# Kernel tuning notes

Measured on AMD Instinct MI355X. Metric: run time of the kernel, lower is better.

The kernel has to match this reference:

```python
import jax, jax.numpy as jnp
import numpy as np

MAX_ITER = 10
F_TOL = 1e-8
FREE_NUM = 100  # free_idx[1] + 1
OUT_DIM = 512


def setup_inputs() -> dict:
    key = jax.random.key(0)
    ks = jax.random.split(key, 13)
    f32 = jnp.float32
    b = jax.random.normal(ks[0], (64, 448), f32)
    # MLP params (nn.Linear convention: W [out, in], bias [out])
    W1 = jax.random.normal(ks[1], (1024, 448), f32) * 0.05
    b1 = jax.random.normal(ks[2], (1024,), f32) * 0.01
    W2 = jax.random.normal(ks[3], (1024, 1024), f32) * 0.03
    b2 = jax.random.normal(ks[4], (1024,), f32) * 0.01
    W3 = jax.random.normal(ks[5], (1024, 1024), f32) * 0.03
    b3 = jax.random.normal(ks[6], (1024,), f32) * 0.01
    W4 = jax.random.normal(ks[7], (512, 1024), f32) * 0.03
    b4 = jax.random.normal(ks[8], (512,), f32) * 0.01
    A = jax.random.normal(ks[9], (448, 512), f32) * 0.05
    WzProj = jax.random.normal(ks[10], (512, 512), f32) * 0.01  # contractive
    WbProj = jax.random.normal(ks[11], (512, 448), f32) * 0.05
    return {"b": b, "W1": W1, "b1": b1, "W2": W2, "b2": b2, "W3": W3,
            "b3": b3, "W4": W4, "b4": b4, "A": A, "WzProj": WzProj,
            "WbProj": WbProj}


def _projection(out, b0, A, WzProj, WbProj):
    # Fixed-point projection with on-device convergence flag + Jacobian accum
    bsz = out.shape[0]
    Bias = b0 @ WbProj.T                     # [bsz, d]
    col = jnp.arange(OUT_DIM)
    J0 = jnp.broadcast_to(jnp.eye(OUT_DIM, dtype=out.dtype),
                          (bsz, OUT_DIM, OUT_DIM))
    def cond(st):
        _, _, it, done = st
        return (it <= MAX_ITER) & (~done)
    def body(st):
        z, J, it, _ = st
        z = Bias + z @ WzProj.T
        # rows to clamp: negative AND in the ReLU (non-free) block
        mask = (z < 0) & (col >= FREE_NUM)                 # [bsz, d]
        J_iter = jnp.where(mask[:, :, None], 0.0, WzProj[None])  # [bsz,d,d]
        J = jnp.einsum('bij,bjk->bik', J_iter, J)          # bmm
        z = jnp.where(mask, 0.0, z)                        # u, relu(v)
        worst = jnp.max(jnp.abs(z @ A.T - b0))             # inf-norm residual
        return (z, J, it + 1, worst <= F_TOL)
    z, J, _, _ = jax.lax.while_loop(
        cond, body, (out, J0, jnp.int32(1), jnp.array(False)))
    return z, J


def reference(b, W1, b1, W2, b2, W3, b3, W4, b4, A, WzProj, WbProj):
    b0 = b
    h = b  # truncate_idx = [0, 448] -> full slice
    h = jax.nn.relu(h @ W1.T + b1)
    h = jax.nn.relu(h @ W2.T + b2)
    h = jax.nn.relu(h @ W3.T + b3)
    out = h @ W4.T + b4                                    # [bsz, 512]
    z_star, _ = _projection(out, b0, A, WzProj, WbProj)
    return (z_star, out)
```

## Files before the change

kernel.cpp:

```cpp
#include <hip/hip_runtime.h>


#define FREE0 100

__global__ __launch_bounds__(256) void transpose512(
    const float* __restrict__ Wz, float* __restrict__ WzT)
{
    __shared__ __align__(16) float Ts[64][65];
    const int t  = threadIdx.x;
    const int k0 = (blockIdx.x >> 3) * 64;
    const int n0 = (blockIdx.x & 7) * 64;
    #pragma unroll
    for (int i = 0; i < 4; ++i) {
        int f  = i * 256 + t;
        int r  = f >> 4;
        int c4 = (f & 15) << 2;
        const float4 v =
            *reinterpret_cast<const float4*>(Wz + (n0 + r) * 512 + k0 + c4);
        Ts[c4 + 0][r] = v.x; Ts[c4 + 1][r] = v.y;
        Ts[c4 + 2][r] = v.z; Ts[c4 + 3][r] = v.w;
    }
    __syncthreads();
    #pragma unroll
    for (int i = 0; i < 4; ++i) {
        int f   = i * 256 + t;
        int kk  = f >> 4;
        int nn4 = (f & 15) << 2;
        float4 w;
        w.x = Ts[kk][nn4 + 0]; w.y = Ts[kk][nn4 + 1];
        w.z = Ts[kk][nn4 + 2]; w.w = Ts[kk][nn4 + 3];
        *reinterpret_cast<float4*>(WzT + (k0 + kk) * 512 + n0 + nn4) = w;
    }
}

template <bool PRE>
__global__ __launch_bounds__(256) void linear44(
    const float* __restrict__ X,
    const float* __restrict__ bp,
    const float* __restrict__ W,
    float* __restrict__ Cp,
    int N, int K)
{
    __shared__ __align__(16) float Xs[64][68];
    __shared__ __align__(16) float Ws[64][68];

    const int t  = threadIdx.x;
    const int n0 = blockIdx.x * 64;
    const int kb = blockIdx.y * 64;

    for (int f = t; f < 4096; f += 256) {
        const int a  = f >> 6;
        const int kk = f & 63;
        float xv = X[a * K + kb + kk];
        if (PRE) xv = fmaxf(xv + bp[kb + kk], 0.f);
        Xs[kk][a] = xv;
        Ws[kk][a] = W[(n0 + a) * K + kb + kk];
    }
    __syncthreads();

    const int rg = t & 15;
    const int cg = t >> 4;

    float4 acc0 = {0,0,0,0}, acc1 = {0,0,0,0};
    float4 acc2 = {0,0,0,0}, acc3 = {0,0,0,0};

    #pragma unroll 16
    for (int kk = 0; kk < 64; ++kk) {
        const float4 xv = *reinterpret_cast<const float4*>(&Xs[kk][rg * 4]);
        const float4 wv = *reinterpret_cast<const float4*>(&Ws[kk][cg * 4]);
        acc0.x = fmaf(xv.x, wv.x, acc0.x);
        acc0.y = fmaf(xv.x, wv.y, acc0.y);
        acc0.z = fmaf(xv.x, wv.z, acc0.z);
        acc0.w = fmaf(xv.x, wv.w, acc0.w);
        acc1.x = fmaf(xv.y, wv.x, acc1.x);
        acc1.y = fmaf(xv.y, wv.y, acc1.y);
        acc1.z = fmaf(xv.y, wv.z, acc1.z);
        acc1.w = fmaf(xv.y, wv.w, acc1.w);
        acc2.x = fmaf(xv.z, wv.x, acc2.x);
        acc2.y = fmaf(xv.z, wv.y, acc2.y);
        acc2.z = fmaf(xv.z, wv.z, acc2.z);
        acc2.w = fmaf(xv.z, wv.w, acc2.w);
        acc3.x = fmaf(xv.w, wv.x, acc3.x);
        acc3.y = fmaf(xv.w, wv.y, acc3.y);
        acc3.z = fmaf(xv.w, wv.z, acc3.z);
        acc3.w = fmaf(xv.w, wv.w, acc3.w);
    }

    float* c0 = Cp + (rg * 4 + 0) * N + n0 + cg * 4;
    float* c1 = Cp + (rg * 4 + 1) * N + n0 + cg * 4;
    float* c2 = Cp + (rg * 4 + 2) * N + n0 + cg * 4;
    float* c3 = Cp + (rg * 4 + 3) * N + n0 + cg * 4;
    atomicAdd(c0 + 0, acc0.x); atomicAdd(c0 + 1, acc0.y);
    atomicAdd(c0 + 2, acc0.z); atomicAdd(c0 + 3, acc0.w);
    atomicAdd(c1 + 0, acc1.x); atomicAdd(c1 + 1, acc1.y);
    atomicAdd(c1 + 2, acc1.z); atomicAdd(c1 + 3, acc1.w);
    atomicAdd(c2 + 0, acc2.x); atomicAdd(c2 + 1, acc2.y);
    atomicAdd(c2 + 2, acc2.z); atomicAdd(c2 + 3, acc2.w);
    atomicAdd(c3 + 0, acc3.x); atomicAdd(c3 + 1, acc3.y);
    atomicAdd(c3 + 2, acc3.z); atomicAdd(c3 + 3, acc3.w);
}

__global__ __launch_bounds__(1024, 4) void zloopf(
    const float* __restrict__ pre4,
    const float* __restrict__ b4,
    const float* __restrict__ WzT,
    const float* __restrict__ bz,
    float* __restrict__ dout)
{
    __shared__ float part[20][2][512];
    __shared__ float zs[512][2];

    const int t   = threadIdx.x;
    const int bid = blockIdx.x;
    const int r   = t >> 9;
    const int c   = t & 511;
    const int row = bid * 2 + r;

    const float z0 = pre4[row * 512 + c] + b4[c];
    dout[32768 + row * 512 + c] = z0;
    zs[c][r] = z0;
    const float biasv = bz[row * 512 + c];
    __syncthreads();

    const int wv = t >> 6;
    const int l  = t & 63;
    const float* wbase = WzT + (wv * 32) * 512 + l * 8;

    for (int it = 0; it < 10; ++it) {
        float4 a00 = {0,0,0,0}, a01 = {0,0,0,0};
        float4 a10 = {0,0,0,0}, a11 = {0,0,0,0};
        const float* wp = wbase;
        #pragma unroll 8
        for (int kk = 0; kk < 32; ++kk) {
            const float4 w0 = *reinterpret_cast<const float4*>(wp);
            const float4 w1 = *reinterpret_cast<const float4*>(wp + 4);
            const float2 zr =
                *reinterpret_cast<const float2*>(&zs[wv * 32 + kk][0]);
            a00.x = fmaf(zr.x, w0.x, a00.x);
            a00.y = fmaf(zr.x, w0.y, a00.y);
            a00.z = fmaf(zr.x, w0.z, a00.z);
            a00.w = fmaf(zr.x, w0.w, a00.w);
            a01.x = fmaf(zr.x, w1.x, a01.x);
            a01.y = fmaf(zr.x, w1.y, a01.y);
            a01.z = fmaf(zr.x, w1.z, a01.z);
            a01.w = fmaf(zr.x, w1.w, a01.w);
            a10.x = fmaf(zr.y, w0.x, a10.x);
            a10.y = fmaf(zr.y, w0.y, a10.y);
            a10.z = fmaf(zr.y, w0.z, a10.z);
            a10.w = fmaf(zr.y, w0.w, a10.w);
            a11.x = fmaf(zr.y, w1.x, a11.x);
            a11.y = fmaf(zr.y, w1.y, a11.y);
            a11.z = fmaf(zr.y, w1.z, a11.z);
            a11.w = fmaf(zr.y, w1.w, a11.w);
            wp += 512;
        }
        *reinterpret_cast<float4*>(&part[wv][0][l * 8    ]) = a00;
        *reinterpret_cast<float4*>(&part[wv][0][l * 8 + 4]) = a01;
        *reinterpret_cast<float4*>(&part[wv][1][l * 8    ]) = a10;
        *reinterpret_cast<float4*>(&part[wv][1][l * 8 + 4]) = a11;
        __syncthreads();

        float v = biasv;
        #pragma unroll
        for (int w = 0; w < 16; ++w) v += part[w][r][c];
        if (c >= FREE0) v = fmaxf(v, 0.f);
        zs[c][r] = v;
        if (it == 9) dout[row * 512 + c] = v;
        __syncthreads();
    }
}

extern "C" void kernel_launch(void* const* d_in, const int* in_sizes, int n_in,
                              void* d_out_v, int out_size, void* d_ws,
                              size_t ws_size, hipStream_t stream)
{
    const float* b  = (const float*)d_in[0];
    const float* W1 = (const float*)d_in[1];
    const float* b1 = (const float*)d_in[2];
    const float* W2 = (const float*)d_in[3];
    const float* b2 = (const float*)d_in[4];
    const float* W3 = (const float*)d_in[5];
    const float* b3 = (const float*)d_in[6];
    const float* W4 = (const float*)d_in[7];
    const float* b4 = (const float*)d_in[8];
    const float* Wz = (const float*)d_in[10];
    const float* Wb = (const float*)d_in[11];

    float* out = (float*)d_out_v;
    float* f   = (float*)d_ws;
    float* WzT  = f;  f += 512 * 512;
    float* zb   = f;
    float* h1   = f;  f += 64 * 1024;
    float* h2   = f;  f += 64 * 1024;
    float* h3   = f;  f += 64 * 1024;
    float* outp = f;  f += 64 * 512;
    float* bzv  = f;  f += 64 * 512;

    hipMemsetAsync(zb, 0, 262144 * sizeof(float), stream);
    transpose512<<<64, 256, 0, stream>>>(Wz, WzT);

    linear44<false><<<dim3(16,  7), 256, 0, stream>>>(b,  nullptr, W1, h1,
                                                      1024, 448);
    linear44<false><<<dim3( 8,  7), 256, 0, stream>>>(b,  nullptr, Wb, bzv,
                                                      512, 448);
    linear44<true ><<<dim3(16, 16), 256, 0, stream>>>(h1, b1, W2, h2,
                                                      1024, 1024);
    linear44<true ><<<dim3(16, 16), 256, 0, stream>>>(h2, b2, W3, h3,
                                                      1024, 1024);
    linear44<true ><<<dim3( 8, 16), 256, 0, stream>>>(h3, b3, W4, outp,
                                                      512, 1024);

    zloopf<<<32, 1024, 0, stream>>>(outp, b4, WzT, bzv, out);
}
```

Baseline: 248.3 us.

## Replace atomic split-K accumulation with partial buffers and reduction kernels

Split-K GEMM blocks now write their partial tiles to separate slices with plain float4 stores instead of scalar atomicAdds, and small reduce kernels (or the z-loop prologue) sum the slices. This removes the workspace memset and the atomic traffic, at the cost of extra launches and more partial-buffer memory traffic. The tile loads are vectorised to float4 reads with transposed shared-memory stores. The z-loop weight loads are batched eight at a time to raise memory-level parallelism.

New measurement: 479.1 us. 1.93x slower.

```diff
diff --git a/kernel.cpp b/kernel.cpp
--- a/kernel.cpp
+++ b/kernel.cpp
@@ -38,7 +38,7 @@
     const float* __restrict__ X,
     const float* __restrict__ bp,
     const float* __restrict__ W,
-    float* __restrict__ Cp,
+    float* __restrict__ P,
     int N, int K)
 {
     __shared__ __align__(16) float Xs[64][68];
@@ -48,13 +48,26 @@
     const int n0 = blockIdx.x * 64;
     const int kb = blockIdx.y * 64;
 
-    for (int f = t; f < 4096; f += 256) {
-        const int a  = f >> 6;
-        const int kk = f & 63;
-        float xv = X[a * K + kb + kk];
-        if (PRE) xv = fmaxf(xv + bp[kb + kk], 0.f);
-        Xs[kk][a] = xv;
-        Ws[kk][a] = W[(n0 + a) * K + kb + kk];
+    #pragma unroll
+    for (int i = 0; i < 4; ++i) {
+        const int f   = i * 256 + t;
+        const int row = f >> 4;
+        const int c4  = (f & 15) << 2;
+        float4 xv = *reinterpret_cast<const float4*>(X + row * K + kb + c4);
+        if (PRE) {
+            const float4 bv =
+                *reinterpret_cast<const float4*>(bp + kb + c4);
+            xv.x = fmaxf(xv.x + bv.x, 0.f);
+            xv.y = fmaxf(xv.y + bv.y, 0.f);
+            xv.z = fmaxf(xv.z + bv.z, 0.f);
+            xv.w = fmaxf(xv.w + bv.w, 0.f);
+        }
+        Xs[c4 + 0][row] = xv.x; Xs[c4 + 1][row] = xv.y;
+        Xs[c4 + 2][row] = xv.z; Xs[c4 + 3][row] = xv.w;
+        const float4 wv =
+            *reinterpret_cast<const float4*>(W + (n0 + row) * K + kb + c4);
+        Ws[c4 + 0][row] = wv.x; Ws[c4 + 1][row] = wv.y;
+        Ws[c4 + 2][row] = wv.z; Ws[c4 + 3][row] = wv.w;
     }
     __syncthreads();
 
@@ -86,28 +99,62 @@
         acc3.w = fmaf(xv.w, wv.w, acc3.w);
     }
 
-    float* c0 = Cp + (rg * 4 + 0) * N + n0 + cg * 4;
-    float* c1 = Cp + (rg * 4 + 1) * N + n0 + cg * 4;
-    float* c2 = Cp + (rg * 4 + 2) * N + n0 + cg * 4;
-    float* c3 = Cp + (rg * 4 + 3) * N + n0 + cg * 4;
-    atomicAdd(c0 + 0, acc0.x); atomicAdd(c0 + 1, acc0.y);
-    atomicAdd(c0 + 2, acc0.z); atomicAdd(c0 + 3, acc0.w);
-    atomicAdd(c1 + 0, acc1.x); atomicAdd(c1 + 1, acc1.y);
-    atomicAdd(c1 + 2, acc1.z); atomicAdd(c1 + 3, acc1.w);
-    atomicAdd(c2 + 0, acc2.x); atomicAdd(c2 + 1, acc2.y);
-    atomicAdd(c2 + 2, acc2.z); atomicAdd(c2 + 3, acc2.w);
-    atomicAdd(c3 + 0, acc3.x); atomicAdd(c3 + 1, acc3.y);
-    atomicAdd(c3 + 2, acc3.z); atomicAdd(c3 + 3, acc3.w);
-}
-
-__global__ __launch_bounds__(1024, 4) void zloopf(
-    const float* __restrict__ pre4,
+    float* base = P + (size_t)blockIdx.y * (64 * N) + n0 + cg * 4;
+    *reinterpret_cast<float4*>(base + (rg * 4 + 0) * N) = acc0;
+    *reinterpret_cast<float4*>(base + (rg * 4 + 1) * N) = acc1;
+    *reinterpret_cast<float4*>(base + (rg * 4 + 2) * N) = acc2;
+    *reinterpret_cast<float4*>(base + (rg * 4 + 3) * N) = acc3;
+}
+
+__global__ __launch_bounds__(256) void reduceS(
+    const float* __restrict__ P, float* __restrict__ out, int len4, int S)
+{
+    const int i = blockIdx.x * 256 + threadIdx.x;
+    if (i >= len4) return;
+    const float4* p4 = reinterpret_cast<const float4*>(P);
+    float4 s = p4[i];
+    for (int j = 1; j < S; ++j) {
+        const float4 v = p4[j * len4 + i];
+        s.x += v.x; s.y += v.y; s.z += v.z; s.w += v.w;
+    }
+    reinterpret_cast<float4*>(out)[i] = s;
+}
+
+#define ZLD(i)                                                              \
+    const float4 wa##i = *reinterpret_cast<const float4*>(wp + (i) * 512);  \
+    const float4 wb##i =                                                    \
+        *reinterpret_cast<const float4*>(wp + (i) * 512 + 4);
+
+#define ZSTEP(i)                                                            \
+    {                                                                       \
+        const float2 zr = *reinterpret_cast<const float2*>(                 \
+            &zs[wv * 32 + blk * 8 + (i)][0]);                               \
+        a00.x = fmaf(zr.x, wa##i.x, a00.x);                                 \
+        a00.y = fmaf(zr.x, wa##i.y, a00.y);                                 \
+        a00.z = fmaf(zr.x, wa##i.z, a00.z);                                 \
+        a00.w = fmaf(zr.x, wa##i.w, a00.w);                                 \
+        a01.x = fmaf(zr.x, wb##i.x, a01.x);                                 \
+        a01.y = fmaf(zr.x, wb##i.y, a01.y);                                 \
+        a01.z = fmaf(zr.x, wb##i.z, a01.z);                                 \
+        a01.w = fmaf(zr.x, wb##i.w, a01.w);                                 \
+        a10.x = fmaf(zr.y, wa##i.x, a10.x);                                 \
+        a10.y = fmaf(zr.y, wa##i.y, a10.y);                                 \
+        a10.z = fmaf(zr.y, wa##i.z, a10.z);                                 \
+        a10.w = fmaf(zr.y, wa##i.w, a10.w);                                 \
+        a11.x = fmaf(zr.y, wb##i.x, a11.x);                                 \
+        a11.y = fmaf(zr.y, wb##i.y, a11.y);                                 \
+        a11.z = fmaf(zr.y, wb##i.z, a11.z);                                 \
+        a11.w = fmaf(zr.y, wb##i.w, a11.w);                                 \
+    }
+
+__global__ __launch_bounds__(1024, 4) void zloopb(
+    const float* __restrict__ P4,
     const float* __restrict__ b4,
     const float* __restrict__ WzT,
-    const float* __restrict__ bz,
+    const float* __restrict__ PWb,
     float* __restrict__ dout)
 {
-    __shared__ float part[20][2][512];
+    __shared__ float part[16][2][512];
     __shared__ float zs[512][2];
 
     const int t   = threadIdx.x;
@@ -115,11 +162,16 @@
     const int r   = t >> 9;
     const int c   = t & 511;
     const int row = bid * 2 + r;
-
-    const float z0 = pre4[row * 512 + c] + b4[c];
-    dout[32768 + row * 512 + c] = z0;
+    const int off = row * 512 + c;
+
+    float z0 = b4[c];
+    #pragma unroll
+    for (int s = 0; s < 16; ++s) z0 += P4[s * 32768 + off];
+    float biasv = 0.f;
+    #pragma unroll
+    for (int s = 0; s < 7; ++s) biasv += PWb[s * 32768 + off];
+    dout[32768 + off] = z0;
     zs[c][r] = z0;
-    const float biasv = bz[row * 512 + c];
     __syncthreads();
 
     const int wv = t >> 6;
@@ -129,30 +181,12 @@
     for (int it = 0; it < 10; ++it) {
         float4 a00 = {0,0,0,0}, a01 = {0,0,0,0};
         float4 a10 = {0,0,0,0}, a11 = {0,0,0,0};
-        const float* wp = wbase;
-        #pragma unroll 8
-        for (int kk = 0; kk < 32; ++kk) {
-            const float4 w0 = *reinterpret_cast<const float4*>(wp);
-            const float4 w1 = *reinterpret_cast<const float4*>(wp + 4);
-            const float2 zr =
-                *reinterpret_cast<const float2*>(&zs[wv * 32 + kk][0]);
-            a00.x = fmaf(zr.x, w0.x, a00.x);
-            a00.y = fmaf(zr.x, w0.y, a00.y);
-            a00.z = fmaf(zr.x, w0.z, a00.z);
-            a00.w = fmaf(zr.x, w0.w, a00.w);
-            a01.x = fmaf(zr.x, w1.x, a01.x);
-            a01.y = fmaf(zr.x, w1.y, a01.y);
-            a01.z = fmaf(zr.x, w1.z, a01.z);
-            a01.w = fmaf(zr.x, w1.w, a01.w);
-            a10.x = fmaf(zr.y, w0.x, a10.x);
-            a10.y = fmaf(zr.y, w0.y, a10.y);
-            a10.z = fmaf(zr.y, w0.z, a10.z);
-            a10.w = fmaf(zr.y, w0.w, a10.w);
-            a11.x = fmaf(zr.y, w1.x, a11.x);
-            a11.y = fmaf(zr.y, w1.y, a11.y);
-            a11.z = fmaf(zr.y, w1.z, a11.z);
-            a11.w = fmaf(zr.y, w1.w, a11.w);
-            wp += 512;
+        #pragma unroll
+        for (int blk = 0; blk < 4; ++blk) {
+            const float* wp = wbase + (blk * 8) * 512;
+            ZLD(0) ZLD(1) ZLD(2) ZLD(3) ZLD(4) ZLD(5) ZLD(6) ZLD(7)
+            ZSTEP(0) ZSTEP(1) ZSTEP(2) ZSTEP(3)
+            ZSTEP(4) ZSTEP(5) ZSTEP(6) ZSTEP(7)
         }
         *reinterpret_cast<float4*>(&part[wv][0][l * 8    ]) = a00;
         *reinterpret_cast<float4*>(&part[wv][0][l * 8 + 4]) = a01;
@@ -165,7 +199,7 @@
         for (int w = 0; w < 16; ++w) v += part[w][r][c];
         if (c >= FREE0) v = fmaxf(v, 0.f);
         zs[c][r] = v;
-        if (it == 9) dout[row * 512 + c] = v;
+        if (it == 9) dout[off] = v;
         __syncthreads();
     }
 }
@@ -188,27 +222,29 @@
 
     float* out = (float*)d_out_v;
     float* f   = (float*)d_ws;
-    float* WzT  = f;  f += 512 * 512;
-    float* zb   = f;
-    float* h1   = f;  f += 64 * 1024;
-    float* h2   = f;  f += 64 * 1024;
-    float* h3   = f;  f += 64 * 1024;
-    float* outp = f;  f += 64 * 512;
-    float* bzv  = f;  f += 64 * 512;
-
-    hipMemsetAsync(zb, 0, 262144 * sizeof(float), stream);
+    float* WzT = f;  f += 262144;
+    float* P   = f;  f += 16 * 65536;
+    float* P4  = f;  f += 16 * 32768;
+    float* PWb = f;  f += 7 * 32768;
+    float* h1  = f;  f += 65536;
+    float* h2  = f;  f += 65536;
+    float* h3  = f;  f += 65536;
+
     transpose512<<<64, 256, 0, stream>>>(Wz, WzT);
 
-    linear44<false><<<dim3(16,  7), 256, 0, stream>>>(b,  nullptr, W1, h1,
+    linear44<false><<<dim3(16,  7), 256, 0, stream>>>(b,  nullptr, W1, P,
                                                       1024, 448);
-    linear44<false><<<dim3( 8,  7), 256, 0, stream>>>(b,  nullptr, Wb, bzv,
+    reduceS<<<64, 256, 0, stream>>>(P, h1, 16384, 7);
+    linear44<false><<<dim3( 8,  7), 256, 0, stream>>>(b,  nullptr, Wb, PWb,
                                                       512, 448);
-    linear44<true ><<<dim3(16, 16), 256, 0, stream>>>(h1, b1, W2, h2,
+    linear44<true ><<<dim3(16, 16), 256, 0, stream>>>(h1, b1, W2, P,
                                                       1024, 1024);
-    linear44<true ><<<dim3(16, 16), 256, 0, stream>>>(h2, b2, W3, h3,
+    reduceS<<<64, 256, 0, stream>>>(P, h2, 16384, 16);
+    linear44<true ><<<dim3(16, 16), 256, 0, stream>>>(h2, b2, W3, P,
                                                       1024, 1024);
-    linear44<true ><<<dim3( 8, 16), 256, 0, stream>>>(h3, b3, W4, outp,
+    reduceS<<<64, 256, 0, stream>>>(P, h3, 16384, 16);
+    linear44<true ><<<dim3( 8, 16), 256, 0, stream>>>(h3, b3, W4, P4,
                                                       512, 1024);
 
-    zloopf<<<32, 1024, 0, stream>>>(outp, b4, WzT, bzv, out);
-}
+    zloopb<<<32, 1024, 0, stream>>>(P4, b4, WzT, PWb, out);
+}
```
